# Kernel optimization log

Measured on AMD Instinct MI355X. Metric: run time of the kernel, lower is better.

Reference implementation:

```python
import jax, jax.numpy as jnp
import numpy as np

N_RAYS = 131072
N_NODES = 524288
ENC_DEPTH = 8
ENC_DIM = 16
N_POINTS = 8
IN_DIM = N_POINTS * ENC_DEPTH * ENC_DIM  # 1024
INNER = 64


def setup_inputs() -> dict:
    key = jax.random.key(0)
    ks = jax.random.split(key, 9)
    orig = jax.random.uniform(ks[0], (N_RAYS, 3), dtype=jnp.float32)
    end = jax.random.uniform(ks[1], (N_RAYS, 3), dtype=jnp.float32)
    history = jax.random.randint(ks[2], (N_RAYS, ENC_DEPTH), 0, N_NODES, dtype=jnp.int32).astype(jnp.int64)
    nodes_min = jax.random.uniform(ks[3], (N_NODES, 3), dtype=jnp.float32)
    # extents strictly positive (module replaces 0 extents with 0.5)
    nodes_extent = jax.random.uniform(ks[4], (N_NODES, 3), dtype=jnp.float32) + 0.1
    emb = jax.random.normal(ks[5], (N_NODES, 8 * ENC_DIM), dtype=jnp.float32) * 0.1
    W1 = jax.random.normal(ks[6], (IN_DIM, INNER), dtype=jnp.float32) * (1.0 / np.sqrt(IN_DIM))
    W2 = jax.random.normal(ks[7], (INNER, INNER), dtype=jnp.float32) * (1.0 / np.sqrt(INNER))
    W3 = jax.random.normal(ks[8], (INNER, 2), dtype=jnp.float32) * (1.0 / np.sqrt(INNER))
    return {"orig": orig, "end": end, "history": history, "nodes_min": nodes_min,
            "nodes_extent": nodes_extent, "emb": emb, "W1": W1, "W2": W2, "W3": W3}


def _net_forward(orig, end, history, nodes_min, nodes_extent, emb, W1, W2, W3):
    n = orig.shape[0]
    d = history.shape[1]
    # gather per-ray, per-depth node data (irregular access)
    nmin = nodes_min[history]          # (n, d, 3)
    ext = nodes_extent[history]        # (n, d, 3)
    po = jnp.clip((orig[:, None, :] - nmin) / ext, 0.0, 1.0)  # (n, d, 3)
    pe = jnp.clip((end[:, None, :] - nmin) / ext, 0.0, 1.0)
    ts = jnp.linspace(0.0, 1.0, N_POINTS, dtype=orig.dtype)
    pts = po[:, :, None, :] + (pe - po)[:, :, None, :] * ts[None, None, :, None]  # (n, d, P, 3)
    xd, yd, zd = pts[..., 0], pts[..., 1], pts[..., 2]
    # corner weights in the same order as bbox_feature.chunk(8): 000,100,010,001,101,011,110,111
    w = jnp.stack([
        (1 - xd) * (1 - yd) * (1 - zd),
        xd * (1 - yd) * (1 - zd),
        (1 - xd) * yd * (1 - zd),
        (1 - xd) * (1 - yd) * zd,
        xd * (1 - yd) * zd,
        (1 - xd) * yd * zd,
        xd * yd * (1 - zd),
        xd * yd * zd,
    ], axis=-1)                                    # (n, d, P, 8)
    corners = emb[history].reshape(n, d, 8, ENC_DIM)  # (n, d, 8, F)
    feat = jnp.einsum('ndpk,ndkf->ndpf', w, corners)  # (n, d, P, F)
    feat = feat.reshape(n, d * N_POINTS * ENC_DIM)    # concat over depth
    h = jax.nn.relu(feat @ W1)
    h = jax.nn.relu(h @ W2)
    a = h @ W3                                        # (n, 2)
    lengths = jnp.linalg.norm(end - orig, axis=-1)
    pred_cls = a[:, 0]
    pred_dist = a[:, 1] * lengths
    return jnp.stack([pred_cls, pred_dist], axis=-1)  # (n, 2)


def reference(orig, end, history, nodes_min, nodes_extent, emb, W1, W2, W3):
    return _net_forward(orig, end, history, nodes_min, nodes_extent, emb, W1, W2, W3)
```

## Files before the change

kernel.cpp:

```cpp
#include <hip/hip_runtime.h>
#include <cstdint>

#define ENC_DEPTH 8
#define RAYS 64
#define THREADS 256

typedef __attribute__((ext_vector_type(8))) short bf16x8;
typedef __attribute__((ext_vector_type(4))) float f32x4;

__device__ __forceinline__ unsigned short f2bf(float x) {
    union { float f; unsigned u; } v; v.f = x;
    unsigned r = v.u + 0x7fffu + ((v.u >> 16) & 1u);
    return (unsigned short)(r >> 16);
}
__device__ __forceinline__ float clamp01(float x) {
    return fminf(fmaxf(x, 0.0f), 1.0f);
}
__device__ __forceinline__ void async_copy16(const float* g, void* l) {
    __builtin_amdgcn_global_load_lds(
        (const __attribute__((address_space(1))) void*)g,
        (__attribute__((address_space(3))) void*)l, 16, 0, 0);
}

__global__ void w1_frag_kernel(const float* __restrict__ W1,
                               unsigned short* __restrict__ W1F) {
    int slot = blockIdx.x * 256 + threadIdx.x;
    int lane = slot & 63, tile = (slot >> 6) & 3, kk = (slot >> 8) & 3, d = slot >> 10;
    int n = tile * 16 + (lane & 15);
    int kbase = d * 128 + kk * 32 + (lane >> 4) * 8;
    bf16x8 v;
    #pragma unroll
    for (int j = 0; j < 8; ++j) v[j] = (short)f2bf(W1[(size_t)(kbase + j) * 64 + n]);
    *(bf16x8*)(W1F + (size_t)slot * 8) = v;
}

__global__ __launch_bounds__(THREADS) void nbvh2(
    const float* __restrict__ orig, const float* __restrict__ endp,
    const int* __restrict__ hist, const float* __restrict__ nodes_min,
    const float* __restrict__ nodes_extent, const float* __restrict__ emb,
    const unsigned short* __restrict__ W1F, const float* __restrict__ W2,
    const float* __restrict__ W3, float* __restrict__ out)
{
    __shared__ __align__(16) float cbuf[2][8320];
    __shared__ float pope_s[RAYS * ENC_DEPTH * 6];
    __shared__ int hist_s[RAYS * ENC_DEPTH];

    const int t = threadIdx.x;
    const int lane = t & 63, w = t >> 6;
    const int r0 = blockIdx.x * RAYS;

    hist_s[t] = hist[r0 * ENC_DEPTH + t];
    hist_s[t + 256] = hist[r0 * ENC_DEPTH + t + 256];
    __syncthreads();

    {
        #pragma unroll
        for (int r = 0; r < 8; ++r) {
            int ray = r * 8 + w * 2 + (lane >> 5);
            int node = hist_s[(ray << 3) + 0];
            const float* g = emb + ((size_t)node << 7) + ((lane & 31) << 2);
            char* l = (char*)(&cbuf[0][0]) + (r * 4 + w) * 1040 + lane * 16;
            async_copy16(g, l);
        }
    }

    #pragma unroll
    for (int rep = 0; rep < 2; ++rep) {
        int task = t + rep * 256;
        int ray = task >> 3;
        int node = hist_s[task];
        float nm0 = nodes_min[node * 3 + 0], nm1 = nodes_min[node * 3 + 1], nm2 = nodes_min[node * 3 + 2];
        float ex0 = nodes_extent[node * 3 + 0], ex1 = nodes_extent[node * 3 + 1], ex2 = nodes_extent[node * 3 + 2];
        float o0 = orig[(r0 + ray) * 3 + 0], o1 = orig[(r0 + ray) * 3 + 1], o2 = orig[(r0 + ray) * 3 + 2];
        float e0 = endp[(r0 + ray) * 3 + 0], e1 = endp[(r0 + ray) * 3 + 1], e2 = endp[(r0 + ray) * 3 + 2];
        float* pp = pope_s + task * 6;
        pp[0] = clamp01((o0 - nm0) / ex0);
        pp[1] = clamp01((o1 - nm1) / ex1);
        pp[2] = clamp01((o2 - nm2) / ex2);
        pp[3] = clamp01((e0 - nm0) / ex0);
        pp[4] = clamp01((e1 - nm1) / ex1);
        pp[5] = clamp01((e2 - nm2) / ex2);
    }
    __syncthreads();

    f32x4 acc[4];
    #pragma unroll
    for (int i = 0; i < 4; ++i) acc[i] = (f32x4){0.f, 0.f, 0.f, 0.f};

    const int c = lane & 15, q = lane >> 4;
    const int ray = w * 16 + c;
    const int qh = q & 1;
    const int qp = q >> 1;

    #pragma unroll 1
    for (int d = 0; d < ENC_DEPTH; ++d) {
        if (d < ENC_DEPTH - 1) {
            float* dst = &cbuf[(d + 1) & 1][0];
            #pragma unroll
            for (int r = 0; r < 8; ++r) {
                int rr = r * 8 + w * 2 + (lane >> 5);
                int node = hist_s[(rr << 3) + d + 1];
                const float* g = emb + ((size_t)node << 7) + ((lane & 31) << 2);
                char* l = (char*)dst + (r * 4 + w) * 1040 + lane * 16;
                async_copy16(g, l);
            }
        }

        bf16x8 bfr[4][4];
        #pragma unroll
        for (int kk = 0; kk < 4; ++kk)
            #pragma unroll
            for (int tile = 0; tile < 4; ++tile)
                bfr[kk][tile] = *(const bf16x8*)(W1F +
                    ((size_t)(((d * 4 + kk) * 4 + tile) * 64 + lane)) * 8);

        const float* pp = pope_s + ((ray << 3) + d) * 6;
        float po0 = pp[0], po1 = pp[1], po2 = pp[2], pe0 = pp[3], pe1 = pp[4], pe2 = pp[5];
        float X[4], OX[4], Y[4], OY[4], Z[4], OZ[4];
        #pragma unroll
        for (int kk = 0; kk < 4; ++kk) {
            float tp = (float)(2 * kk + qp) * (1.0f / 7.0f);
            X[kk] = po0 + (pe0 - po0) * tp; OX[kk] = 1.f - X[kk];
            Y[kk] = po1 + (pe1 - po1) * tp; OY[kk] = 1.f - Y[kk];
            Z[kk] = po2 + (pe2 - po2) * tp; OZ[kk] = 1.f - Z[kk];
        }

        float fa[4][8];
        #pragma unroll
        for (int kk = 0; kk < 4; ++kk)
            #pragma unroll
            for (int j = 0; j < 8; ++j) fa[kk][j] = 0.f;

        const float* crow = &cbuf[d & 1][0] + (ray >> 1) * 260 + (ray & 1) * 128 + (qh << 3);
        #pragma unroll
        for (int c8 = 0; c8 < 8; ++c8) {
            float4 ea = *(const float4*)(crow + c8 * 16);
            float4 eb = *(const float4*)(crow + c8 * 16 + 4);
            #pragma unroll
            for (int kk = 0; kk < 4; ++kk) {
                float wx = ((0xD2 >> c8) & 1) ? X[kk] : OX[kk];
                float wy = ((0xE4 >> c8) & 1) ? Y[kk] : OY[kk];
                float wz = ((0xB8 >> c8) & 1) ? Z[kk] : OZ[kk];
                float wgt = wx * wy * wz;
                fa[kk][0] = fmaf(wgt, ea.x, fa[kk][0]);
                fa[kk][1] = fmaf(wgt, ea.y, fa[kk][1]);
                fa[kk][2] = fmaf(wgt, ea.z, fa[kk][2]);
                fa[kk][3] = fmaf(wgt, ea.w, fa[kk][3]);
                fa[kk][4] = fmaf(wgt, eb.x, fa[kk][4]);
                fa[kk][5] = fmaf(wgt, eb.y, fa[kk][5]);
                fa[kk][6] = fmaf(wgt, eb.z, fa[kk][6]);
                fa[kk][7] = fmaf(wgt, eb.w, fa[kk][7]);
            }
        }

        #pragma unroll
        for (int kk = 0; kk < 4; ++kk) {
            bf16x8 af;
            #pragma unroll
            for (int j = 0; j < 8; ++j) af[j] = (short)f2bf(fa[kk][j]);
            #pragma unroll
            for (int tile = 0; tile < 4; ++tile)
                acc[tile] = __builtin_amdgcn_mfma_f32_16x16x32_bf16(af, bfr[kk][tile], acc[tile], 0, 0, 0);
        }
        __syncthreads();
    }

    float* h1 = &cbuf[0][0];
    #pragma unroll
    for (int tile = 0; tile < 4; ++tile)
        #pragma unroll
        for (int r = 0; r < 4; ++r)
            h1[(w * 16 + q * 4 + r) * 68 + tile * 16 + c] = fmaxf(acc[tile][r], 0.f);
    __syncthreads();

    float* h2 = &cbuf[1][0];
    {
        int ray2 = t >> 2, jg = (t & 3) << 4;
        float s[16];
        #pragma unroll
        for (int j = 0; j < 16; ++j) s[j] = 0.f;
        const float* hrow = h1 + ray2 * 68;
        #pragma unroll 4
        for (int i = 0; i < 64; ++i) {
            float hv = hrow[i];
            const float4* wr = (const float4*)(W2 + (i << 6) + jg);
            float4 a0 = wr[0], a1 = wr[1], a2 = wr[2], a3 = wr[3];
            s[0]  = fmaf(hv, a0.x, s[0]);  s[1]  = fmaf(hv, a0.y, s[1]);
            s[2]  = fmaf(hv, a0.z, s[2]);  s[3]  = fmaf(hv, a0.w, s[3]);
            s[4]  = fmaf(hv, a1.x, s[4]);  s[5]  = fmaf(hv, a1.y, s[5]);
            s[6]  = fmaf(hv, a1.z, s[6]);  s[7]  = fmaf(hv, a1.w, s[7]);
            s[8]  = fmaf(hv, a2.x, s[8]);  s[9]  = fmaf(hv, a2.y, s[9]);
            s[10] = fmaf(hv, a2.z, s[10]); s[11] = fmaf(hv, a2.w, s[11]);
            s[12] = fmaf(hv, a3.x, s[12]); s[13] = fmaf(hv, a3.y, s[13]);
            s[14] = fmaf(hv, a3.z, s[14]); s[15] = fmaf(hv, a3.w, s[15]);
        }
        float* h2row = h2 + ray2 * 68 + jg;
        #pragma unroll
        for (int j = 0; j < 16; ++j) h2row[j] = fmaxf(s[j], 0.f);
    }
    __syncthreads();

    if (t < 128) {
        int ray3 = t >> 1, cc = t & 1;
        const float* hrow = h2 + ray3 * 68;
        float a = 0.f;
        #pragma unroll 16
        for (int i = 0; i < 64; ++i) a = fmaf(hrow[i], W3[i * 2 + cc], a);
        if (cc) {
            float dx = endp[(r0 + ray3) * 3 + 0] - orig[(r0 + ray3) * 3 + 0];
            float dy = endp[(r0 + ray3) * 3 + 1] - orig[(r0 + ray3) * 3 + 1];
            float dz = endp[(r0 + ray3) * 3 + 2] - orig[(r0 + ray3) * 3 + 2];
            a *= sqrtf(dx * dx + dy * dy + dz * dz);
        }
        out[((r0 + ray3) << 1) + cc] = a;
    }
}

extern "C" void kernel_launch(void* const* d_in, const int* in_sizes, int n_in,
                              void* d_out, int out_size, void* d_ws, size_t ws_size,
                              hipStream_t stream) {
    const float* orig = (const float*)d_in[0];
    const float* endp = (const float*)d_in[1];
    const int*   hist = (const int*)d_in[2];
    const float* nmin = (const float*)d_in[3];
    const float* next = (const float*)d_in[4];
    const float* emb  = (const float*)d_in[5];
    const float* W1   = (const float*)d_in[6];
    const float* W2   = (const float*)d_in[7];
    const float* W3   = (const float*)d_in[8];
    float* out = (float*)d_out;
    unsigned short* W1F = (unsigned short*)d_ws;

    w1_frag_kernel<<<dim3(32), dim3(256), 0, stream>>>(W1, W1F);

    const int n_rays = in_sizes[0] / 3;
    nbvh2<<<dim3(n_rays / RAYS), dim3(THREADS), 0, stream>>>(
        orig, endp, hist, nmin, next, emb, W1F, W2, W3, out);
}
```

Baseline: 546.3 us.

## Convert embedding table to bf16 per call to halve gather traffic

After: 601.1 us. 1.1x slower.

```diff
diff --git a/kernel.cpp b/kernel.cpp
--- a/kernel.cpp
+++ b/kernel.cpp
@@ -1,5 +1,6 @@
 #include <hip/hip_runtime.h>
 #include <cstdint>
+#include <type_traits>
 
 #define ENC_DEPTH 8
 #define RAYS 64
@@ -13,13 +14,30 @@
     unsigned r = v.u + 0x7fffu + ((v.u >> 16) & 1u);
     return (unsigned short)(r >> 16);
 }
+__device__ __forceinline__ float bf2f(unsigned short h) {
+    union { unsigned u; float f; } v; v.u = ((unsigned)h) << 16;
+    return v.f;
+}
 __device__ __forceinline__ float clamp01(float x) {
     return fminf(fmaxf(x, 0.0f), 1.0f);
 }
-__device__ __forceinline__ void async_copy16(const float* g, void* l) {
+__device__ __forceinline__ void async_copy16(const void* g, void* l) {
     __builtin_amdgcn_global_load_lds(
         (const __attribute__((address_space(1))) void*)g,
         (__attribute__((address_space(3))) void*)l, 16, 0, 0);
+}
+
+__global__ void emb_bf16_kernel(const float* __restrict__ emb,
+                                unsigned short* __restrict__ emb2) {
+    size_t i = ((size_t)blockIdx.x * 256 + threadIdx.x) * 8;
+    float4 a = *(const float4*)(emb + i);
+    float4 b = *(const float4*)(emb + i + 4);
+    bf16x8 v;
+    v[0] = (short)f2bf(a.x); v[1] = (short)f2bf(a.y);
+    v[2] = (short)f2bf(a.z); v[3] = (short)f2bf(a.w);
+    v[4] = (short)f2bf(b.x); v[5] = (short)f2bf(b.y);
+    v[6] = (short)f2bf(b.z); v[7] = (short)f2bf(b.w);
+    *(bf16x8*)(emb2 + i) = v;
 }
 
 __global__ void w1_frag_kernel(const float* __restrict__ W1,
@@ -34,14 +52,16 @@
     *(bf16x8*)(W1F + (size_t)slot * 8) = v;
 }
 
-__global__ __launch_bounds__(THREADS) void nbvh2(
+template <int BF16T>
+__global__ __launch_bounds__(THREADS) void nbvh3(
     const float* __restrict__ orig, const float* __restrict__ endp,
     const int* __restrict__ hist, const float* __restrict__ nodes_min,
-    const float* __restrict__ nodes_extent, const float* __restrict__ emb,
+    const float* __restrict__ nodes_extent, const void* __restrict__ embx,
     const unsigned short* __restrict__ W1F, const float* __restrict__ W2,
     const float* __restrict__ W3, float* __restrict__ out)
 {
-    __shared__ __align__(16) float cbuf[2][8320];
+    using CTy = typename std::conditional<BF16T, unsigned short, float>::type;
+    __shared__ __align__(16) CTy cbuf[2][8320];
     __shared__ float pope_s[RAYS * ENC_DEPTH * 6];
     __shared__ int hist_s[RAYS * ENC_DEPTH];
 
@@ -53,16 +73,28 @@
     hist_s[t + 256] = hist[r0 * ENC_DEPTH + t + 256];
     __syncthreads();
 
-    {
-        #pragma unroll
-        for (int r = 0; r < 8; ++r) {
-            int ray = r * 8 + w * 2 + (lane >> 5);
-            int node = hist_s[(ray << 3) + 0];
-            const float* g = emb + ((size_t)node << 7) + ((lane & 31) << 2);
-            char* l = (char*)(&cbuf[0][0]) + (r * 4 + w) * 1040 + lane * 16;
-            async_copy16(g, l);
-        }
-    }
+    auto issue_gather = [&](int d, int buf) {
+        char* base = (char*)&cbuf[buf][0];
+        if (BF16T) {
+            #pragma unroll
+            for (int r = 0; r < 4; ++r) {
+                int ray = r * 16 + w * 4 + (lane >> 4);
+                int node = hist_s[(ray << 3) + d];
+                const char* g = (const char*)embx + ((size_t)node << 8) + ((lane & 15) << 4);
+                async_copy16(g, base + (r * 4 + w) * 1040 + lane * 16);
+            }
+        } else {
+            #pragma unroll
+            for (int r = 0; r < 8; ++r) {
+                int ray = r * 8 + w * 2 + (lane >> 5);
+                int node = hist_s[(ray << 3) + d];
+                const char* g = (const char*)embx + ((size_t)node << 9) + ((lane & 31) << 4);
+                async_copy16(g, base + (r * 4 + w) * 1040 + lane * 16);
+            }
+        }
+    };
+
+    issue_gather(0, 0);
 
     #pragma unroll
     for (int rep = 0; rep < 2; ++rep) {
@@ -94,17 +126,7 @@
 
     #pragma unroll 1
     for (int d = 0; d < ENC_DEPTH; ++d) {
-        if (d < ENC_DEPTH - 1) {
-            float* dst = &cbuf[(d + 1) & 1][0];
-            #pragma unroll
-            for (int r = 0; r < 8; ++r) {
-                int rr = r * 8 + w * 2 + (lane >> 5);
-                int node = hist_s[(rr << 3) + d + 1];
-                const float* g = emb + ((size_t)node << 7) + ((lane & 31) << 2);
-                char* l = (char*)dst + (r * 4 + w) * 1040 + lane * 16;
-                async_copy16(g, l);
-            }
-        }
+        if (d < ENC_DEPTH - 1) issue_gather(d + 1, (d + 1) & 1);
 
         bf16x8 bfr[4][4];
         #pragma unroll
@@ -131,25 +153,33 @@
             #pragma unroll
             for (int j = 0; j < 8; ++j) fa[kk][j] = 0.f;
 
-        const float* crow = &cbuf[d & 1][0] + (ray >> 1) * 260 + (ray & 1) * 128 + (qh << 3);
-        #pragma unroll
-        for (int c8 = 0; c8 < 8; ++c8) {
-            float4 ea = *(const float4*)(crow + c8 * 16);
-            float4 eb = *(const float4*)(crow + c8 * 16 + 4);
+        #pragma unroll
+        for (int j = 0; j < 8; ++j) {
+            int c8 = j ^ (c & 3);
+            float e[8];
+            if (BF16T) {
+                const unsigned short* crow = (const unsigned short*)&cbuf[d & 1][0]
+                    + (ray >> 2) * 520 + (ray & 3) * 128 + c8 * 16 + qh * 8;
+                bf16x8 cv = *(const bf16x8*)crow;
+                #pragma unroll
+                for (int i = 0; i < 8; ++i) e[i] = bf2f((unsigned short)cv[i]);
+            } else {
+                const float* crow = (const float*)&cbuf[d & 1][0]
+                    + (ray >> 1) * 260 + (ray & 1) * 128 + c8 * 16 + qh * 8;
+                float4 ea = *(const float4*)crow;
+                float4 eb = *(const float4*)(crow + 4);
+                e[0] = ea.x; e[1] = ea.y; e[2] = ea.z; e[3] = ea.w;
+                e[4] = eb.x; e[5] = eb.y; e[6] = eb.z; e[7] = eb.w;
+            }
             #pragma unroll
             for (int kk = 0; kk < 4; ++kk) {
                 float wx = ((0xD2 >> c8) & 1) ? X[kk] : OX[kk];
                 float wy = ((0xE4 >> c8) & 1) ? Y[kk] : OY[kk];
                 float wz = ((0xB8 >> c8) & 1) ? Z[kk] : OZ[kk];
                 float wgt = wx * wy * wz;
-                fa[kk][0] = fmaf(wgt, ea.x, fa[kk][0]);
-                fa[kk][1] = fmaf(wgt, ea.y, fa[kk][1]);
-                fa[kk][2] = fmaf(wgt, ea.z, fa[kk][2]);
-                fa[kk][3] = fmaf(wgt, ea.w, fa[kk][3]);
-                fa[kk][4] = fmaf(wgt, eb.x, fa[kk][4]);
-                fa[kk][5] = fmaf(wgt, eb.y, fa[kk][5]);
-                fa[kk][6] = fmaf(wgt, eb.z, fa[kk][6]);
-                fa[kk][7] = fmaf(wgt, eb.w, fa[kk][7]);
+                #pragma unroll
+                for (int i = 0; i < 8; ++i)
+                    fa[kk][i] = fmaf(wgt, e[i], fa[kk][i]);
             }
         }
 
@@ -165,21 +195,21 @@
         __syncthreads();
     }
 
-    float* h1 = &cbuf[0][0];
+    float* h1 = (float*)&cbuf[0][0];
+    float* h2 = BF16T ? ((float*)&cbuf[1][0]) : (((float*)&cbuf[0][0]) + 4160);
     #pragma unroll
     for (int tile = 0; tile < 4; ++tile)
         #pragma unroll
         for (int r = 0; r < 4; ++r)
-            h1[(w * 16 + q * 4 + r) * 68 + tile * 16 + c] = fmaxf(acc[tile][r], 0.f);
-    __syncthreads();
-
-    float* h2 = &cbuf[1][0];
+            h1[(w * 16 + q * 4 + r) * 65 + tile * 16 + c] = fmaxf(acc[tile][r], 0.f);
+    __syncthreads();
+
     {
         int ray2 = t >> 2, jg = (t & 3) << 4;
         float s[16];
         #pragma unroll
         for (int j = 0; j < 16; ++j) s[j] = 0.f;
-        const float* hrow = h1 + ray2 * 68;
+        const float* hrow = h1 + ray2 * 65;
         #pragma unroll 4
         for (int i = 0; i < 64; ++i) {
             float hv = hrow[i];
@@ -194,7 +224,7 @@
             s[12] = fmaf(hv, a3.x, s[12]); s[13] = fmaf(hv, a3.y, s[13]);
             s[14] = fmaf(hv, a3.z, s[14]); s[15] = fmaf(hv, a3.w, s[15]);
         }
-        float* h2row = h2 + ray2 * 68 + jg;
+        float* h2row = h2 + ray2 * 65 + jg;
         #pragma unroll
         for (int j = 0; j < 16; ++j) h2row[j] = fmaxf(s[j], 0.f);
     }
@@ -202,7 +232,7 @@
 
     if (t < 128) {
         int ray3 = t >> 1, cc = t & 1;
-        const float* hrow = h2 + ray3 * 68;
+        const float* hrow = h2 + ray3 * 65;
         float a = 0.f;
         #pragma unroll 16
         for (int i = 0; i < 64; ++i) a = fmaf(hrow[i], W3[i * 2 + cc], a);
@@ -229,11 +259,23 @@
     const float* W2   = (const float*)d_in[7];
     const float* W3   = (const float*)d_in[8];
     float* out = (float*)d_out;
-    unsigned short* W1F = (unsigned short*)d_ws;
-
-    w1_frag_kernel<<<dim3(32), dim3(256), 0, stream>>>(W1, W1F);
-
+
+    const int n_nodes = in_sizes[5] / 128;
+    const size_t emb2_bytes = (size_t)n_nodes * 128 * 2;
     const int n_rays = in_sizes[0] / 3;
-    nbvh2<<<dim3(n_rays / RAYS), dim3(THREADS), 0, stream>>>(
-        orig, endp, hist, nmin, next, emb, W1F, W2, W3, out);
-}
+    const bool use_bf16 = ws_size >= emb2_bytes + 131072 * 2;
+
+    if (use_bf16) {
+        unsigned short* EMB2 = (unsigned short*)d_ws;
+        unsigned short* W1F = (unsigned short*)((char*)d_ws + emb2_bytes);
+        emb_bf16_kernel<<<dim3((n_nodes * 128) / (256 * 8)), dim3(256), 0, stream>>>(emb, EMB2);
+        w1_frag_kernel<<<dim3(32), dim3(256), 0, stream>>>(W1, W1F);
+        nbvh3<1><<<dim3(n_rays / RAYS), dim3(THREADS), 0, stream>>>(
+            orig, endp, hist, nmin, next, EMB2, W1F, W2, W3, out);
+    } else {
+        unsigned short* W1F = (unsigned short*)d_ws;
+        w1_frag_kernel<<<dim3(32), dim3(256), 0, stream>>>(W1, W1F);
+        nbvh3<0><<<dim3(n_rays / RAYS), dim3(THREADS), 0, stream>>>(
+            orig, endp, hist, nmin, next, emb, W1F, W2, W3, out);
+    }
+}
```
